# Kernel optimization log

Hardware: AMD Instinct MI355X
Metric: run time of the kernel (lower is better)

Reference implementation:

```python
import jax, jax.numpy as jnp
import numpy as np

B = 128; DIM_IN = 3; MAX_CYCLE = 50; NODES = 18
T = MAX_CYCLE * NODES          # cycle_size = 900
F1, F2 = 32, 64                # stgcn_filters
NCLS = 3
N = B * T                      # nodes seen by GATv2 = 115200
E = 12 * N                     # edges (avg degree 12)
EPS = 1e-5


def setup_inputs() -> dict:
    key = jax.random.key(0)
    keys = iter(jax.random.split(key, 48))
    def p(shape, scale=0.05):
        return jax.random.normal(next(keys), shape, jnp.float32) * scale
    inp = {}
    inp["x"] = jax.random.normal(next(keys), (B, DIM_IN, T), jnp.float32)
    inp["edge_index"] = jax.random.randint(next(keys), (2, E), 0, N)
    def block(pfx, cin, c):
        inp[pfx + "_tc1_w"] = p((c, cin, 5)); inp[pfx + "_tc1_b"] = p((c,))
        inp[pfx + "_wl"] = p((c, c)); inp[pfx + "_bl"] = p((c,))
        inp[pfx + "_wr"] = p((c, c)); inp[pfx + "_br"] = p((c,))
        inp[pfx + "_att"] = p((c,)); inp[pfx + "_gbias"] = p((c,))
        inp[pfx + "_bn_g"] = jnp.ones((c,), jnp.float32)
        inp[pfx + "_bn_b"] = jnp.zeros((c,), jnp.float32)
        inp[pfx + "_tc2_w"] = p((c, c, 5)); inp[pfx + "_tc2_b"] = p((c,))
    block("b1", DIM_IN, F1)
    block("b2", F1, F2)
    inp["fc1_w"] = p((128, T * F2), 0.01); inp["fc1_b"] = p((128,))
    inp["hbn1_g"] = jnp.ones((128,), jnp.float32); inp["hbn1_b"] = jnp.zeros((128,), jnp.float32)
    inp["fc2_w"] = p((64, 128)); inp["fc2_b"] = p((64,))
    inp["hbn2_g"] = jnp.ones((64,), jnp.float32); inp["hbn2_b"] = jnp.zeros((64,), jnp.float32)
    inp["fc3_w"] = p((NCLS, 64)); inp["fc3_b"] = p((NCLS,))
    return inp


def _conv1d_same(x, w, b):
    # x: [B, Cin, T], w: [Cout, Cin, 5], 'same' padding (pad 2/2)
    y = jax.lax.conv_general_dilated(x, w, (1,), [(2, 2)],
                                     dimension_numbers=("NCH", "OIH", "NCH"))
    return y + b[None, :, None]


def _bn(h, g, b):
    # BatchNorm1d on [N, C] with batch statistics
    m = h.mean(0)
    v = h.var(0)
    return (h - m) * jax.lax.rsqrt(v + EPS) * g + b


def _gatv2(h, src, dst, wl, bl, wr, br, att, gbias):
    # PyG GATv2Conv, heads=1, negative_slope=0.2, self loops already in src/dst
    xl = h @ wl.T + bl            # source transform, also the message
    xr = h @ wr.T + br            # target transform
    e = jnp.dot(jax.nn.leaky_relu(xl[src] + xr[dst], 0.2), att)  # [E]
    m = jax.ops.segment_max(e, dst, num_segments=N)
    ex = jnp.exp(e - m[dst])
    s = jax.ops.segment_sum(ex, dst, num_segments=N)
    alpha = ex / s[dst]
    out = jax.ops.segment_sum(alpha[:, None] * xl[src], dst, num_segments=N)
    return out + gbias


def _block(x, src, dst, tc1_w, tc1_b, wl, bl, wr, br, att, gbias, bn_g, bn_b, tc2_w, tc2_b):
    x = jax.nn.relu(_conv1d_same(x, tc1_w, tc1_b))      # [B, C, T]
    C = tc1_w.shape[0]
    h = x.reshape(T * B, C)                             # torch .view(T*B, C) (raw row-major)
    h = jax.nn.relu(_gatv2(h, src, dst, wl, bl, wr, br, att, gbias))
    h = _bn(h, bn_g, bn_b)
    h = h.reshape(B, C, T)                              # torch .view(B, C, T)
    return jax.nn.relu(_conv1d_same(h, tc2_w, tc2_b))


def reference(x, edge_index,
              b1_tc1_w, b1_tc1_b, b1_wl, b1_bl, b1_wr, b1_br, b1_att, b1_gbias,
              b1_bn_g, b1_bn_b, b1_tc2_w, b1_tc2_b,
              b2_tc1_w, b2_tc1_b, b2_wl, b2_bl, b2_wr, b2_br, b2_att, b2_gbias,
              b2_bn_g, b2_bn_b, b2_tc2_w, b2_tc2_b,
              fc1_w, fc1_b, hbn1_g, hbn1_b, fc2_w, fc2_b, hbn2_g, hbn2_b, fc3_w, fc3_b):
    sl = jnp.arange(N, dtype=edge_index.dtype)          # PyG add_self_loops=True
    src = jnp.concatenate([edge_index[0], sl])
    dst = jnp.concatenate([edge_index[1], sl])
    h = _block(x, src, dst, b1_tc1_w, b1_tc1_b, b1_wl, b1_bl, b1_wr, b1_br,
               b1_att, b1_gbias, b1_bn_g, b1_bn_b, b1_tc2_w, b1_tc2_b)
    h = jax.nn.relu(h)                                  # extra relu on non-final block (dropout off)
    h = _block(h, src, dst, b2_tc1_w, b2_tc1_b, b2_wl, b2_bl, b2_wr, b2_br,
               b2_att, b2_gbias, b2_bn_g, b2_bn_b, b2_tc2_w, b2_tc2_b)
    h = h.reshape(B, F2 * T)
    h = jax.nn.relu(h @ fc1_w.T + fc1_b)
    h = _bn(h, hbn1_g, hbn1_b)
    h = jax.nn.relu(h @ fc2_w.T + fc2_b)
    h = _bn(h, hbn2_g, hbn2_b)
    logits = h @ fc3_w.T + fc3_b
    return (jax.nn.sigmoid(logits), logits)
```

## Files before the change

kernel.cpp:

```cpp
#include <hip/hip_runtime.h>
#include <hip/hip_bf16.h>

typedef __hip_bfloat16 bf16;
typedef __attribute__((ext_vector_type(8))) short s16x8;
typedef __attribute__((ext_vector_type(4))) float f32x4;
#define DEV static __device__ __forceinline__

DEV float b2f(bf16 v){ return __bfloat162float(v); }
DEV bf16  f2b(float v){ return __float2bfloat16(v); }
DEV int   is_f32(const void* gones){ return ((const unsigned int*)gones)[0] == 0x3F800000u ? 1 : 0; }
DEV float ldin(const void* p, int f32, int i){
    return f32 ? ((const float*)p)[i] : __bfloat162float(((const bf16*)p)[i]);
}
DEV void unpk(unsigned u, float& a, float& b){
    a = __uint_as_float(u << 16);
    b = __uint_as_float(u & 0xffff0000u);
}
DEV float lrelu(float t){ return fmaxf(t, 0.f) + 0.2f * fminf(t, 0.f); }
DEV unsigned short bfu(float v){ bf16 h = f2b(v); return *(unsigned short*)&h; }

constexpr int Bb  = 128;
constexpr int Tt  = 900;
constexpr int Nn  = Bb * Tt;
constexpr int Ee  = 12 * Nn;
constexpr int CAP = 48;
constexpr int NBK  = 256;
constexpr int NPB  = Nn / NBK;
constexpr int BCAP = 8192;
constexpr int WROWS = 96 + 1024 + 2048 + 4096;
constexpr int WTOT  = WROWS * 5;
constexpr int WBF   = 5120 + 10240 + 20480;

__global__ __launch_bounds__(256) void k_wprep(const void* wa, const void* wb_, const void* wc,
    const void* wd, const void* gones, float* __restrict__ wp, bf16* __restrict__ wbf,
    int* __restrict__ gcur){
    const int f32 = is_f32(gones);
    if (blockIdx.x == 0 && threadIdx.x < NBK) gcur[threadIdx.x] = 0;
    int e = blockIdx.x * 256 + threadIdx.x;
    if (e < WTOT){
        int r = e / 5, k = e - r * 5;
        const void* src; int rb;
        if (r < 96)      { src = wa; rb = 0; }
        else if (r < 1120){ src = wb_; rb = 96; }
        else if (r < 3168){ src = wc; rb = 1120; }
        else             { src = wd; rb = 3168; }
        wp[r * 8 + k] = ldin(src, f32, (r - rb) * 5 + k);
    } else if (e < WTOT + WBF){
        int e2 = e - WTOT;
        const void* src; int kk, r;
        if (e2 < 5120)      { kk = e2 >> 10; r = e2 & 1023; src = wb_; }
        else if (e2 < 15360){ int e3 = e2 - 5120;  kk = e3 >> 11; r = e3 & 2047; src = wc; }
        else                { int e3 = e2 - 15360; kk = e3 >> 12; r = e3 & 4095; src = wd; }
        wbf[e2] = f2b(ldin(src, f32, r * 5 + kk));
    }
}

__global__ __launch_bounds__(256) void k_bucket(const int* __restrict__ ei,
                                                int* __restrict__ gcur, int2* __restrict__ bkt){
    constexpr int TILE = 4096;
    const int base = blockIdx.x * TILE;
    const int tid = threadIdx.x;
    __shared__ int cnt[NBK];
    __shared__ int gbase[NBK];
    cnt[tid] = 0;
    __syncthreads();
    int es[16], er[16], eb[16], rk[16];
    #pragma unroll
    for (int k = 0; k < 16; ++k){
        int idx = base + k * 256 + tid;
        if (idx < Ee){
            es[k] = ei[idx];
            int d = ei[Ee + idx];
            eb[k] = d / NPB;
            er[k] = d - eb[k] * NPB;
            rk[k] = atomicAdd(&cnt[eb[k]], 1);
        } else eb[k] = -1;
    }
    __syncthreads();
    {
        int c = cnt[tid];
        gbase[tid] = (c > 0) ? atomicAdd(&gcur[tid], c) : 0;
    }
    __syncthreads();
    #pragma unroll
    for (int k = 0; k < 16; ++k){
        if (eb[k] >= 0){
            int slot = gbase[eb[k]] + rk[k];
            if (slot < BCAP)
                bkt[(size_t)eb[k] * BCAP + slot] = make_int2(er[k], es[k]);
        }
    }
}

__global__ __launch_bounds__(256) void k_csr2(const int2* __restrict__ bkt, const int* __restrict__ gcur,
                                              int* __restrict__ csr, int* __restrict__ cnt){
    const int b = blockIdx.x;
    const int n0 = b * NPB;
    __shared__ int lcnt[NPB];
    for (int i = threadIdx.x; i < NPB; i += 256) lcnt[i] = 0;
    __syncthreads();
    const int tot = min(gcur[b], BCAP);
    for (int i = threadIdx.x; i < tot; i += 256){
        int2 e = bkt[(size_t)b * BCAP + i];
        int p = atomicAdd(&lcnt[e.x], 1);
        if (p < CAP) csr[(size_t)(n0 + e.x) * CAP + p] = e.y;
    }
    __syncthreads();
    for (int i = threadIdx.x; i < NPB; i += 256) cnt[n0 + i] = lcnt[i];
}

template<bool EXT, int CIN, int COUT, bool BN>
__global__ __launch_bounds__(256) void k_conv(const void* __restrict__ x,
    const float* __restrict__ wp, int wbase,
    const void* __restrict__ bias, const float* __restrict__ scale, const float* __restrict__ shift,
    const void* __restrict__ gones, float* __restrict__ y)
{
    const int f32 = is_f32(gones);
    __shared__ alignas(16) float xs[CIN][132];
    const int b = blockIdx.x >> 3, t0 = (blockIdx.x & 7) * 128;
    const int tid = threadIdx.x;
    for (int i = tid; i < CIN * 132; i += 256){
        int ci = i / 132, tt = i % 132;
        int gt = t0 + tt - 2;
        float v = 0.f;
        if (gt >= 0 && gt < Tt){
            int idx = (b * CIN + ci) * Tt + gt;
            v = EXT ? ldin(x, f32, idx) : ((const float*)x)[idx];
            if (BN){
                int f = (ci * (Tt % CIN) + gt) % CIN;
                v = v * scale[f] + shift[f];
            }
        }
        xs[ci][tt] = v;
    }
    __syncthreads();
    constexpr int HALF = COUT / 2;
    constexpr int NT   = 256 / HALF;
    constexpr int NW   = 128 / (NT * 4);
    const int cop = tid / NT;
    const int tch = tid % NT;
    const int co = cop, co2 = cop + HALF;
    float acc[NW][2][4];
    #pragma unroll
    for (int iw = 0; iw < NW; ++iw)
        #pragma unroll
        for (int h = 0; h < 2; ++h)
            #pragma unroll
            for (int j = 0; j < 4; ++j) acc[iw][h][j] = 0.f;

    const float* w0p = wp + (size_t)(wbase + co  * CIN) * 8;
    const float* w1p = wp + (size_t)(wbase + co2 * CIN) * 8;
    float4 na = *(const float4*)w0p; float na4 = w0p[4];
    float4 nb = *(const float4*)w1p; float nb4 = w1p[4];
    for (int ci = 0; ci < CIN; ++ci){
        const float w0[5] = {na.x, na.y, na.z, na.w, na4};
        const float w1[5] = {nb.x, nb.y, nb.z, nb.w, nb4};
        if (ci + 1 < CIN){
            const float* p0 = w0p + (size_t)(ci + 1) * 8;
            const float* p1 = w1p + (size_t)(ci + 1) * 8;
            na = *(const float4*)p0; na4 = p0[4];
            nb = *(const float4*)p1; nb4 = p1[4];
        }
        #pragma unroll
        for (int iw = 0; iw < NW; ++iw){
            const int tl = tch * 4 + iw * NT * 4;
            float4 a  = *(const float4*)&xs[ci][tl];
            float4 bq = *(const float4*)&xs[ci][tl + 4];
            float xw[8] = {a.x,a.y,a.z,a.w,bq.x,bq.y,bq.z,bq.w};
            #pragma unroll
            for (int k = 0; k < 5; ++k)
                #pragma unroll
                for (int j = 0; j < 4; ++j){
                    acc[iw][0][j] = fmaf(xw[j + k], w0[k], acc[iw][0][j]);
                    acc[iw][1][j] = fmaf(xw[j + k], w1[k], acc[iw][1][j]);
                }
        }
    }
    const float bv0 = ldin(bias, f32, co), bv1 = ldin(bias, f32, co2);
    #pragma unroll
    for (int iw = 0; iw < NW; ++iw){
        const int t = t0 + tch * 4 + iw * NT * 4;
        if (t < Tt){
            float4 o0, o1;
            o0.x = fmaxf(acc[iw][0][0] + bv0, 0.f); o0.y = fmaxf(acc[iw][0][1] + bv0, 0.f);
            o0.z = fmaxf(acc[iw][0][2] + bv0, 0.f); o0.w = fmaxf(acc[iw][0][3] + bv0, 0.f);
            o1.x = fmaxf(acc[iw][1][0] + bv1, 0.f); o1.y = fmaxf(acc[iw][1][1] + bv1, 0.f);
            o1.z = fmaxf(acc[iw][1][2] + bv1, 0.f); o1.w = fmaxf(acc[iw][1][3] + bv1, 0.f);
            *(float4*)&y[(b * COUT + co ) * Tt + t] = o0;
            *(float4*)&y[(b * COUT + co2) * Tt + t] = o1;
        }
    }
}

template<int CIN, int COUT, bool BN>
__global__ __launch_bounds__(256) void k_convM(const float* __restrict__ x, const bf16* __restrict__ wbf,
    int wbase,
    const void* __restrict__ bias, const float* __restrict__ scale, const float* __restrict__ shift,
    const void* __restrict__ gones, float* __restrict__ y)
{
    const int f32 = is_f32(gones);
    constexpr int STR = CIN + 8;
    constexpr int CI2 = CIN / 2;
    __shared__ alignas(16) float smem[COUT * 132];
    unsigned short* xsT = (unsigned short*)smem;
    const int b = blockIdx.x >> 3, t0 = (blockIdx.x & 7) * 128;
    const int tid = threadIdx.x;
    for (int i = tid; i < CI2 * 128; i += 256){
        int ci2 = i >> 7, tt = i & 127;
        int gt = t0 + tt - 2;
        int ci = ci2 * 2;
        unsigned pack = 0;
        if (gt >= 0 && gt < Tt){
            float v0 = x[(b * CIN + ci) * Tt + gt];
            float v1 = x[(b * CIN + ci + 1) * Tt + gt];
            if (BN){
                int fa = (4 * ci + gt) & (CIN - 1), fb = (4 * ci + 4 + gt) & (CIN - 1);
                v0 = v0 * scale[fa] + shift[fa];
                v1 = v1 * scale[fb] + shift[fb];
            }
            pack = (unsigned)bfu(v0) | ((unsigned)bfu(v1) << 16);
        }
        *(unsigned*)&xsT[tt * STR + ci] = pack;
    }
    if (tid < CI2 * 4){
        int ci2 = tid >> 2, tt = 128 + (tid & 3);
        int gt = t0 + tt - 2;
        int ci = ci2 * 2;
        unsigned pack = 0;
        if (gt < Tt){
            float v0 = x[(b * CIN + ci) * Tt + gt];
            float v1 = x[(b * CIN + ci + 1) * Tt + gt];
            if (BN){
                int fa = (4 * ci + gt) & (CIN - 1), fb = (4 * ci + 4 + gt) & (CIN - 1);
                v0 = v0 * scale[fa] + shift[fa];
                v1 = v1 * scale[fb] + shift[fb];
            }
            pack = (unsigned)bfu(v0) | ((unsigned)bfu(v1) << 16);
        }
        *(unsigned*)&xsT[tt * STR + ci] = pack;
    }
    __syncthreads();
    const int lane = tid & 63, wid = tid >> 6;
    const int l15 = lane & 15, quad = lane >> 4;
    constexpr int MT  = COUT / 16;
    constexpr int NTP = 2 * MT;
    const int mt  = (MT == 4) ? wid : (wid & 1);
    const int ntb = (MT == 4) ? 0 : (wid >> 1) * NTP;
    const int co0 = mt * 16;
    f32x4 acc[NTP];
    #pragma unroll
    for (int nt = 0; nt < NTP; ++nt){ f32x4 z = {0.f, 0.f, 0.f, 0.f}; acc[nt] = z; }
    for (int kk = 0; kk < 5; ++kk){
        #pragma unroll
        for (int kb = 0; kb < CIN / 32; ++kb){
            s16x8 a = *(const s16x8*)&wbf[wbase + kk * (COUT * CIN) + (co0 + l15) * CIN + kb * 32 + quad * 8];
            #pragma unroll
            for (int nt = 0; nt < NTP; ++nt){
                s16x8 bf = *(const s16x8*)&xsT[((ntb + nt) * 16 + l15 + kk) * STR + kb * 32 + quad * 8];
                acc[nt] = __builtin_amdgcn_mfma_f32_16x16x32_bf16(a, bf, acc[nt], 0, 0, 0);
            }
        }
    }
    __syncthreads();
    #pragma unroll
    for (int nt = 0; nt < NTP; ++nt)
        #pragma unroll
        for (int r = 0; r < 4; ++r)
            smem[(co0 + quad * 4 + r) * 132 + (ntb + nt) * 16 + l15] = acc[nt][r];
    __syncthreads();
    for (int i = tid; i < COUT * 32; i += 256){
        int co = i >> 5, c4 = (i & 31) << 2;
        int t = t0 + c4;
        if (t < Tt){
            float4 o = *(float4*)&smem[co * 132 + c4];
            float bb = ldin(bias, f32, co);
            o.x = fmaxf(o.x + bb, 0.f); o.y = fmaxf(o.y + bb, 0.f);
            o.z = fmaxf(o.z + bb, 0.f); o.w = fmaxf(o.w + bb, 0.f);
            float* dst = &y[(b * COUT + co) * Tt + t];
            if (t + 3 < Tt) *(float4*)dst = o;
            else {
                float ov[4] = {o.x, o.y, o.z, o.w};
                for (int j = 0; j < 4 && t + j < Tt; ++j) dst[j] = ov[j];
            }
        }
    }
}

template<int C>
__global__ __launch_bounds__(256) void k_xlxr(const float* __restrict__ h,
    const void* __restrict__ wl, const void* __restrict__ bl,
    const void* __restrict__ wr, const void* __restrict__ br,
    const void* __restrict__ gones, unsigned short* __restrict__ xlh, float* __restrict__ xr)
{
    const int f32 = is_f32(gones);
    constexpr int NB = 4096 / C;
    constexpr int HS = NB + 4;
    constexpr int WS = C + 4;
    __shared__ alignas(16) float hT [C][HS];
    __shared__ alignas(16) float wlT[C][WS];
    __shared__ alignas(16) float wrT[C][WS];
    const int tid = threadIdx.x;
    const int n0 = blockIdx.x * NB;
    for (int i = tid; i < NB * C; i += 256){
        int n = i / C, c = i % C;
        hT[c][n] = h[(n0 + n) * C + c];
    }
    for (int i = tid; i < C * C; i += 256){
        int f = i / C, c = i % C;
        wlT[c][f] = ldin(wl, f32, i);
        wrT[c][f] = ldin(wr, f32, i);
    }
    __syncthreads();
    constexpr int FG = C / 4;
    const int fg = tid % FG, ng = tid / FG;
    const int nloc = ng * 4, floc = fg * 4;
    float blv[4], brv[4];
    #pragma unroll
    for (int j = 0; j < 4; ++j){ blv[j] = ldin(bl, f32, floc + j); brv[j] = ldin(br, f32, floc + j); }
    float accL[4][4], accR[4][4];
    #pragma unroll
    for (int i = 0; i < 4; ++i)
        #pragma unroll
        for (int j = 0; j < 4; ++j){ accL[i][j] = 0.f; accR[i][j] = 0.f; }
    for (int c = 0; c < C; ++c){
        float4 hv = *(const float4*)&hT [c][nloc];
        float4 lv = *(const float4*)&wlT[c][floc];
        float4 rv = *(const float4*)&wrT[c][floc];
        float ha[4] = {hv.x,hv.y,hv.z,hv.w};
        float la[4] = {lv.x,lv.y,lv.z,lv.w};
        float ra[4] = {rv.x,rv.y,rv.z,rv.w};
        #pragma unroll
        for (int i = 0; i < 4; ++i)
            #pragma unroll
            for (int j = 0; j < 4; ++j){
                accL[i][j] = fmaf(ha[i], la[j], accL[i][j]);
                accR[i][j] = fmaf(ha[i], ra[j], accR[i][j]);
            }
    }
    #pragma unroll
    for (int i = 0; i < 4; ++i){
        size_t n = n0 + nloc + i;
        bf16 hb[4];
        hb[0] = f2b(accL[i][0] + blv[0]); hb[1] = f2b(accL[i][1] + blv[1]);
        hb[2] = f2b(accL[i][2] + blv[2]); hb[3] = f2b(accL[i][3] + blv[3]);
        *(ushort4*)&xlh[n * C + floc] = *(ushort4*)hb;
        float4 r;
        r.x = accR[i][0] + brv[0]; r.y = accR[i][1] + brv[1];
        r.z = accR[i][2] + brv[2]; r.w = accR[i][3] + brv[3];
        *(float4*)&xr[n * C + floc] = r;
    }
}

template<int L> DEV float rsumL(float v){
    #pragma unroll
    for (int s = L / 2; s > 0; s >>= 1) v += __shfl_xor(v, s, 64);
    return v;
}

template<int C, int FPL>
__global__ __launch_bounds__(256) void k_gat(const unsigned short* __restrict__ xlh,
    const float* __restrict__ xr,
    const int* __restrict__ csr, const int* __restrict__ cnt,
    const void* __restrict__ att, const void* __restrict__ gbias,
    const void* __restrict__ gones, float* __restrict__ out)
{
    const int f32 = is_f32(gones);
    constexpr int L   = C / FPL;
    constexpr int NPW = 64 / L;
    const int lane = threadIdx.x & 63, wid = threadIdx.x >> 6;
    const int sub = lane / L, fp = lane % L;
    const int node = (blockIdx.x * 4 + wid) * NPW + sub;
    const int f0 = FPL * fp;
    float xrv[FPL], attv[FPL];
    if constexpr (FPL == 4){
        float4 t = *(const float4*)&xr[(size_t)node * C + f0];
        xrv[0] = t.x; xrv[1] = t.y; xrv[2] = t.z; xrv[3] = t.w;
    } else {
        float2 t = *(const float2*)&xr[(size_t)node * C + f0];
        xrv[0] = t.x; xrv[1] = t.y;
    }
    #pragma unroll
    for (int i = 0; i < FPL; ++i) attv[i] = ldin(att, f32, f0 + i);
    const int deg = min(cnt[node], CAP);
    int degu = deg;
    degu = max(degu, __shfl_xor(degu, 32, 64));
    degu = max(degu, __shfl_xor(degu, 16, 64));

    auto loadv = [&](int s, float (&v)[FPL]){
        if constexpr (FPL == 4){
            uint2 u = *(const uint2*)&xlh[(size_t)s * C + f0];
            unpk(u.x, v[0], v[1]); unpk(u.y, v[2], v[3]);
        } else {
            unsigned u = *(const unsigned*)&xlh[(size_t)s * C + f0];
            unpk(u, v[0], v[1]);
        }
    };
    auto score = [&](const float (&v)[FPL]){
        float l = lrelu(v[0] + xrv[0]) * attv[0];
        #pragma unroll
        for (int i = 1; i < FPL; ++i) l = fmaf(lrelu(v[i] + xrv[i]), attv[i], l);
        return rsumL<L>(l);
    };

    float ssum, acc[FPL];
    {
        float v[FPL];
        loadv(node, v);
        float w = __expf(score(v));
        ssum = w;
        #pragma unroll
        for (int i = 0; i < FPL; ++i) acc[i] = w * v[i];
    }
    for (int j = 0; j < degu; j += 4){
        int4 s4 = *(const int4*)&csr[(size_t)node * CAP + j];
        const bool a0 = (j + 0 < deg), a1 = (j + 1 < deg), a2 = (j + 2 < deg), a3 = (j + 3 < deg);
        int s0 = a0 ? s4.x : node, s1 = a1 ? s4.y : node;
        int s2 = a2 ? s4.z : node, s3 = a3 ? s4.w : node;
        float v0[FPL], v1[FPL], v2[FPL], v3[FPL];
        loadv(s0, v0); loadv(s1, v1); loadv(s2, v2); loadv(s3, v3);
        float e0 = score(v0), e1 = score(v1), e2 = score(v2), e3 = score(v3);
        float w0 = a0 ? __expf(e0) : 0.f;
        float w1 = a1 ? __expf(e1) : 0.f;
        float w2 = a2 ? __expf(e2) : 0.f;
        float w3 = a3 ? __expf(e3) : 0.f;
        ssum += (w0 + w1) + (w2 + w3);
        #pragma unroll
        for (int i = 0; i < FPL; ++i)
            acc[i] += fmaf(w0, v0[i], w1 * v1[i]) + fmaf(w2, v2[i], w3 * v3[i]);
    }
    float inv = 1.f / ssum;
    if constexpr (FPL == 4){
        float4 o;
        o.x = fmaxf(fmaf(acc[0], inv, ldin(gbias, f32, f0)),     0.f);
        o.y = fmaxf(fmaf(acc[1], inv, ldin(gbias, f32, f0 + 1)), 0.f);
        o.z = fmaxf(fmaf(acc[2], inv, ldin(gbias, f32, f0 + 2)), 0.f);
        o.w = fmaxf(fmaf(acc[3], inv, ldin(gbias, f32, f0 + 3)), 0.f);
        *(float4*)&out[(size_t)node * C + f0] = o;
    } else {
        float2 o;
        o.x = fmaxf(fmaf(acc[0], inv, ldin(gbias, f32, f0)),     0.f);
        o.y = fmaxf(fmaf(acc[1], inv, ldin(gbias, f32, f0 + 1)), 0.f);
        *(float2*)&out[(size_t)node * C + f0] = o;
    }
}

template<int C>
__global__ __launch_bounds__(256) void k_bnstat1(const float* __restrict__ h, double* __restrict__ part){
    const int tid = threadIdx.x;
    double s1 = 0.0, s2 = 0.0;
    const int total = Nn * C;
    for (int idx = blockIdx.x * 256 + tid; idx < total; idx += 65536){
        float v = h[idx];
        s1 += v; s2 += (double)v * v;
    }
    __shared__ double r1[256], r2[256];
    r1[tid] = s1; r2[tid] = s2;
    __syncthreads();
    if (tid < C){
        double a = 0.0, b = 0.0;
        #pragma unroll
        for (int q = 0; q < 256 / C; ++q){ a += r1[tid + q * C]; b += r2[tid + q * C]; }
        part[blockIdx.x * 2 * C + tid]     = a;
        part[blockIdx.x * 2 * C + C + tid] = b;
    }
}

template<int C>
__global__ void k_bnstat2(const double* __restrict__ part, const void* __restrict__ g,
                          const void* __restrict__ b, const void* __restrict__ gones,
                          float* __restrict__ scale, float* __restrict__ shift){
    const int f32 = is_f32(gones);
    const int f = threadIdx.x;
    double s1 = 0.0, s2 = 0.0;
    for (int s = 0; s < 256; ++s){ s1 += part[s * 2 * C + f]; s2 += part[s * 2 * C + C + f]; }
    double mean = s1 / (double)Nn;
    double var  = s2 / (double)Nn - mean * mean;
    float sc = (float)((double)ldin(g, f32, f) / sqrt(var + 1e-5));
    float sh = ldin(b, f32, f) - (float)mean * sc;
    scale[f] = sc; shift[f] = sh;
}

__global__ __launch_bounds__(256) void k_fc1(const float* __restrict__ h, const void* __restrict__ w1,
                                             const void* __restrict__ gones, float* __restrict__ part){
    const int f32 = is_f32(gones);
    __shared__ alignas(16) float AT[32][136];
    __shared__ alignas(16) float BT[32][136];
    const int tid = threadIdx.x;
    const int blk = blockIdx.x;
    const int k0 = blk * 128;
    const int bg = tid >> 4, jg = tid & 15;
    const int row = tid >> 5, kk = tid & 31;
    float ar[16], br[16];
    #pragma unroll
    for (int q = 0; q < 16; ++q){
        int idx = (row + q * 8) * 57600 + k0 + kk;
        ar[q] = h[idx];
        br[q] = ldin(w1, f32, idx);
    }
    float acc[8][8];
    #pragma unroll
    for (int i = 0; i < 8; ++i)
        #pragma unroll
        for (int j = 0; j < 8; ++j) acc[i][j] = 0.f;
    for (int ch = 0; ch < 4; ++ch){
        __syncthreads();
        #pragma unroll
        for (int q = 0; q < 16; ++q){
            AT[kk][row + q * 8] = ar[q];
            BT[kk][row + q * 8] = br[q];
        }
        __syncthreads();
        if (ch < 3){
            const int kb = k0 + (ch + 1) * 32;
            #pragma unroll
            for (int q = 0; q < 16; ++q){
                int idx = (row + q * 8) * 57600 + kb + kk;
                ar[q] = h[idx];
                br[q] = ldin(w1, f32, idx);
            }
        }
        for (int k2 = 0; k2 < 32; ++k2){
            float4 a0 = *(const float4*)&AT[k2][bg * 8];
            float4 a1 = *(const float4*)&AT[k2][bg * 8 + 4];
            float4 c0 = *(const float4*)&BT[k2][jg * 8];
            float4 c1 = *(const float4*)&BT[k2][jg * 8 + 4];
            float av[8] = {a0.x,a0.y,a0.z,a0.w,a1.x,a1.y,a1.z,a1.w};
            float bv[8] = {c0.x,c0.y,c0.z,c0.w,c1.x,c1.y,c1.z,c1.w};
            #pragma unroll
            for (int i = 0; i < 8; ++i)
                #pragma unroll
                for (int j = 0; j < 8; ++j) acc[i][j] = fmaf(av[i], bv[j], acc[i][j]);
        }
    }
    #pragma unroll
    for (int i = 0; i < 8; ++i){
        int bb = bg * 8 + i;
        #pragma unroll
        for (int q = 0; q < 2; ++q){
            float4 o;
            o.x = acc[i][q*4+0]; o.y = acc[i][q*4+1]; o.z = acc[i][q*4+2]; o.w = acc[i][q*4+3];
            *(float4*)&part[blk * 16384 + bb * 128 + jg * 8 + q * 4] = o;
        }
    }
}

__global__ void k_fc1red1(const float* __restrict__ part, float* __restrict__ pr2){
    const int y = blockIdx.x >> 6;
    const int o = (blockIdx.x & 63) * 256 + threadIdx.x;
    const int sb0 = y * 57;
    const int sb1 = min(sb0 + 57, 450);
    float s = 0.f;
    for (int sb = sb0; sb < sb1; ++sb) s += part[(size_t)sb * 16384 + o];
    pr2[(size_t)y * 16384 + o] = s;
}

__global__ void k_fc1red2(const float* __restrict__ pr2, const void* __restrict__ bias,
                          const void* __restrict__ gones, float* __restrict__ out1){
    const int f32 = is_f32(gones);
    const int o = blockIdx.x * 256 + threadIdx.x;
    float s = ldin(bias, f32, o & 127);
    #pragma unroll
    for (int y = 0; y < 8; ++y) s += pr2[(size_t)y * 16384 + o];
    out1[o] = fmaxf(s, 0.f);
}

__global__ void k_hstat(const float* __restrict__ out1, const void* __restrict__ g1,
                        const void* __restrict__ b1, const void* __restrict__ gones,
                        float* __restrict__ sc, float* __restrict__ sh){
    const int f32 = is_f32(gones);
    const int f = threadIdx.x;
    double s1 = 0.0, s2 = 0.0;
    for (int r = 0; r < 128; ++r){ float v = out1[r * 128 + f]; s1 += v; s2 += (double)v * v; }
    double mean = s1 / 128.0, var = s2 / 128.0 - mean * mean;
    float s = (float)((double)ldin(g1, f32, f) / sqrt(var + 1e-5));
    sc[f] = s;
    sh[f] = ldin(b1, f32, f) - (float)mean * s;
}

__global__ __launch_bounds__(256) void k_fc2(const float* __restrict__ out1,
    const float* __restrict__ sc, const float* __restrict__ sh,
    const void* __restrict__ w2, const void* __restrict__ fb2,
    const void* __restrict__ gones, float* __restrict__ f2)
{
    const int f32 = is_f32(gones);
    __shared__ alignas(16) float hs[4 * 128];
    __shared__ alignas(16) float w2s[64 * 132];
    const int tid = threadIdx.x;
    const int b0 = blockIdx.x * 4;
    for (int i = tid; i < 512; i += 256){
        int f = i & 127;
        hs[i] = out1[b0 * 128 + i] * sc[f] + sh[f];
    }
    for (int i = tid; i < 8192; i += 256)
        w2s[(i >> 7) * 132 + (i & 127)] = ldin(w2, f32, i);
    __syncthreads();
    const int b = tid >> 6, o = tid & 63;
    float acc = ldin(fb2, f32, o);
    const float* hp = &hs[b * 128];
    const float* wq = &w2s[o * 132];
    #pragma unroll
    for (int k = 0; k < 128; k += 4){
        float4 hv = *(const float4*)&hp[k];
        float4 wv = *(const float4*)&wq[k];
        acc = fmaf(hv.x, wv.x, acc); acc = fmaf(hv.y, wv.y, acc);
        acc = fmaf(hv.z, wv.z, acc); acc = fmaf(hv.w, wv.w, acc);
    }
    f2[(b0 + b) * 64 + o] = fmaxf(acc, 0.f);
}

__global__ __launch_bounds__(256) void k_head2(const float* __restrict__ f2,
    const void* g2, const void* b2v, const void* w3, const void* fb3,
    const void* gones, void* __restrict__ out)
{
    const int f32 = is_f32(gones);
    __shared__ float fs[8192];
    __shared__ float sc2[64], sh2[64];
    const int tid = threadIdx.x;
    for (int i = tid; i < 8192; i += 256) fs[i] = f2[i];
    __syncthreads();
    if (tid < 64){
        double s1 = 0.0, s2 = 0.0;
        for (int r = 0; r < 128; ++r){ float v = fs[r * 64 + tid]; s1 += v; s2 += (double)v * v; }
        double mean = s1 / 128.0, var = s2 / 128.0 - mean * mean;
        sc2[tid] = (float)((double)ldin(g2, f32, tid) / sqrt(var + 1e-5));
        sh2[tid] = ldin(b2v, f32, tid) - (float)mean * sc2[tid];
    }
    __syncthreads();
    if (tid < 128){
        float hv[64];
        for (int k = 0; k < 64; ++k) hv[k] = fs[tid * 64 + k] * sc2[k] + sh2[k];
        #pragma unroll
        for (int c = 0; c < 3; ++c){
            float acc = ldin(fb3, f32, c);
            for (int k = 0; k < 64; ++k) acc = fmaf(hv[k], ldin(w3, f32, c * 64 + k), acc);
            float sg = 1.f / (1.f + __expf(-acc));
            if (f32){
                ((float*)out)[384 + tid * 3 + c] = acc;
                ((float*)out)[tid * 3 + c] = sg;
            } else {
                ((bf16*)out)[384 + tid * 3 + c] = f2b(acc);
                ((bf16*)out)[tid * 3 + c] = f2b(sg);
            }
        }
    }
}

extern "C" void kernel_launch(void* const* d_in, const int* in_sizes, int n_in,
                              void* d_out, int out_size, void* d_ws, size_t ws_size,
                              hipStream_t stream)
{
    const void* x   = d_in[0];
    const int*  ei  = (const int*)d_in[1];
    const void* b1_tc1_w=d_in[2];  const void* b1_tc1_b=d_in[3];
    const void* b1_wl   =d_in[4];  const void* b1_bl   =d_in[5];
    const void* b1_wr   =d_in[6];  const void* b1_br   =d_in[7];
    const void* b1_att  =d_in[8];  const void* b1_gb   =d_in[9];
    const void* b1_g    =d_in[10]; const void* b1_bt   =d_in[11];
    const void* b1_tc2_w=d_in[12]; const void* b1_tc2_b=d_in[13];
    const void* b2_tc1_w=d_in[14]; const void* b2_tc1_b=d_in[15];
    const void* b2_wl   =d_in[16]; const void* b2_bl   =d_in[17];
    const void* b2_wr   =d_in[18]; const void* b2_br   =d_in[19];
    const void* b2_att  =d_in[20]; const void* b2_gb   =d_in[21];
    const void* b2_g    =d_in[22]; const void* b2_bt   =d_in[23];
    const void* b2_tc2_w=d_in[24]; const void* b2_tc2_b=d_in[25];
    const void* fc1_w=d_in[26]; const void* fc1_b=d_in[27];
    const void* hbn1_g=d_in[28]; const void* hbn1_b=d_in[29];
    const void* fc2_w=d_in[30]; const void* fc2_b=d_in[31];
    const void* hbn2_g=d_in[32]; const void* hbn2_b=d_in[33];
    const void* fc3_w=d_in[34]; const void* fc3_b=d_in[35];
    const void* gones = b1_g;

    float* ws = (float*)d_ws;
    const size_t NC = (size_t)Nn * 64;
    float* buf0 = ws;
    float* buf1 = ws + NC;
    float* buf2 = ws + 2 * NC;
    int*   csr  = (int*)(ws + 3 * NC);
    int*   cnt  = (int*)((char*)csr + (size_t)Nn * CAP * 4);
    double* bnp = (double*)((char*)cnt + (size_t)Nn * 4);
    float* scale = (float*)(bnp + 32768);
    float* shift = scale + 128;
    unsigned short* xlh = (unsigned short*)(shift + 128);
    int*   gcur = (int*)(xlh + (size_t)Nn * 64);
    float* wp   = (float*)(gcur + NBK);
    bf16*  wbf  = (bf16*)(wp + (size_t)WROWS * 8);
    int2*  bkt  = (int2*)buf2;
    float* part = buf0;
    float* out1 = buf2;
    float* pr2  = buf2 + 16384;
    float* f2b_ = pr2 + 8 * 16384;
    float* hsc  = f2b_ + 8192;
    float* hsh  = hsc + 128;

    k_wprep <<<(WTOT + WBF + 255) / 256, 256, 0, stream>>>(b1_tc1_w, b1_tc2_w, b2_tc1_w, b2_tc2_w,
                                                           gones, wp, wbf, gcur);
    k_bucket<<<(Ee + 4095) / 4096, 256, 0, stream>>>(ei, gcur, bkt);
    k_csr2  <<<NBK, 256, 0, stream>>>(bkt, gcur, csr, cnt);

    k_conv<true, 3, 32, false><<<Bb * 8, 256, 0, stream>>>(x, wp, 0, b1_tc1_b, nullptr, nullptr, gones, buf0);
    k_xlxr<32><<<Nn / 128, 256, 0, stream>>>(buf0, b1_wl, b1_bl, b1_wr, b1_br, gones, xlh, buf1);
    k_gat<32, 2><<<Nn / 16, 256, 0, stream>>>(xlh, buf1, csr, cnt, b1_att, b1_gb, gones, buf2);
    k_bnstat1<32><<<256, 256, 0, stream>>>(buf2, bnp);
    k_bnstat2<32><<<1, 32, 0, stream>>>(bnp, b1_g, b1_bt, gones, scale, shift);
    k_convM<32, 32, true><<<Bb * 8, 256, 0, stream>>>(buf2, wbf, 0, b1_tc2_b, scale, shift, gones, buf0);

    k_convM<32, 64, false><<<Bb * 8, 256, 0, stream>>>(buf0, wbf, 5120, b2_tc1_b, nullptr, nullptr, gones, buf1);
    k_xlxr<64><<<Nn / 64, 256, 0, stream>>>(buf1, b2_wl, b2_bl, b2_wr, b2_br, gones, xlh, buf2);
    k_gat<64, 4><<<Nn / 16, 256, 0, stream>>>(xlh, buf2, csr, cnt, b2_att, b2_gb, gones, buf0);
    k_bnstat1<64><<<256, 256, 0, stream>>>(buf0, bnp);
    k_bnstat2<64><<<1, 64, 0, stream>>>(bnp, b2_g, b2_bt, gones, scale, shift);
    k_convM<64, 64, true><<<Bb * 8, 256, 0, stream>>>(buf0, wbf, 15360, b2_tc2_b, scale, shift, gones, buf1);

    k_fc1<<<450, 256, 0, stream>>>(buf1, fc1_w, gones, part);
    k_fc1red1<<<512, 256, 0, stream>>>(part, pr2);
    k_fc1red2<<<64, 256, 0, stream>>>(pr2, fc1_b, gones, out1);
    k_hstat<<<1, 128, 0, stream>>>(out1, hbn1_g, hbn1_b, gones, hsc, hsh);
    k_fc2<<<32, 256, 0, stream>>>(out1, hsc, hsh, fc2_w, fc2_b, gones, f2b_);
    k_head2<<<1, 256, 0, stream>>>(f2b_, hbn2_g, hbn2_b, fc3_w, fc3_b, gones, d_out);
}
```

Measured before the change: 539.9 us.

## Rewrite xl/xr projection as one-node-per-thread with preconverted fp32 weights

The GATv2 source/target projection kernel now gives each thread one node, holds its feature row in registers, and reads the weights from a global fp32 buffer with a wave-uniform access pattern instead of staging transposed tiles in shared memory. The weight-prep kernel gains a section that converts wl/wr/bl/br for both blocks into that buffer, so the per-block dtype checks and shared-memory setup go away. For C=64 the output features are split over two blocks to limit register pressure. The risk is uncoalesced per-thread row loads and stores with a node stride, and a higher register count.

```diff
diff --git a/kernel.cpp b/kernel.cpp
--- a/kernel.cpp
+++ b/kernel.cpp
@@ -30,10 +30,14 @@
 constexpr int WROWS = 96 + 1024 + 2048 + 4096;
 constexpr int WTOT  = WROWS * 5;
 constexpr int WBF   = 5120 + 10240 + 20480;
+constexpr int WXT   = 2*32*32 + 64 + 2*64*64 + 128;
 
 __global__ __launch_bounds__(256) void k_wprep(const void* wa, const void* wb_, const void* wc,
-    const void* wd, const void* gones, float* __restrict__ wp, bf16* __restrict__ wbf,
-    int* __restrict__ gcur){
+    const void* wd,
+    const void* b1wl, const void* b1bl, const void* b1wr, const void* b1br,
+    const void* b2wl, const void* b2bl, const void* b2wr, const void* b2br,
+    const void* gones, float* __restrict__ wp, bf16* __restrict__ wbf,
+    float* __restrict__ wx, int* __restrict__ gcur){
     const int f32 = is_f32(gones);
     if (blockIdx.x == 0 && threadIdx.x < NBK) gcur[threadIdx.x] = 0;
     int e = blockIdx.x * 256 + threadIdx.x;
@@ -52,6 +56,18 @@
         else if (e2 < 15360){ int e3 = e2 - 5120;  kk = e3 >> 11; r = e3 & 2047; src = wc; }
         else                { int e3 = e2 - 15360; kk = e3 >> 12; r = e3 & 4095; src = wd; }
         wbf[e2] = f2b(ldin(src, f32, r * 5 + kk));
+    } else if (e < WTOT + WBF + WXT){
+        int e3 = e - WTOT - WBF;
+        float v;
+        if      (e3 < 1024)  v = ldin(b1wl, f32, e3);
+        else if (e3 < 2048)  v = ldin(b1wr, f32, e3 - 1024);
+        else if (e3 < 2080)  v = ldin(b1bl, f32, e3 - 2048);
+        else if (e3 < 2112)  v = ldin(b1br, f32, e3 - 2080);
+        else if (e3 < 6208)  v = ldin(b2wl, f32, e3 - 2112);
+        else if (e3 < 10304) v = ldin(b2wr, f32, e3 - 6208);
+        else if (e3 < 10368) v = ldin(b2bl, f32, e3 - 10304);
+        else                 v = ldin(b2br, f32, e3 - 10368);
+        wx[e3] = v;
     }
 }
 
@@ -286,68 +302,50 @@
     }
 }
 
-template<int C>
+template<int C, int SPLIT>
 __global__ __launch_bounds__(256) void k_xlxr(const float* __restrict__ h,
-    const void* __restrict__ wl, const void* __restrict__ bl,
-    const void* __restrict__ wr, const void* __restrict__ br,
-    const void* __restrict__ gones, unsigned short* __restrict__ xlh, float* __restrict__ xr)
+    const float* __restrict__ wx, int wxoff,
+    unsigned short* __restrict__ xlh, float* __restrict__ xr)
 {
-    const int f32 = is_f32(gones);
-    constexpr int NB = 4096 / C;
-    constexpr int HS = NB + 4;
-    constexpr int WS = C + 4;
-    __shared__ alignas(16) float hT [C][HS];
-    __shared__ alignas(16) float wlT[C][WS];
-    __shared__ alignas(16) float wrT[C][WS];
-    const int tid = threadIdx.x;
-    const int n0 = blockIdx.x * NB;
-    for (int i = tid; i < NB * C; i += 256){
-        int n = i / C, c = i % C;
-        hT[c][n] = h[(n0 + n) * C + c];
-    }
-    for (int i = tid; i < C * C; i += 256){
-        int f = i / C, c = i % C;
-        wlT[c][f] = ldin(wl, f32, i);
-        wrT[c][f] = ldin(wr, f32, i);
-    }
-    __syncthreads();
-    constexpr int FG = C / 4;
-    const int fg = tid % FG, ng = tid / FG;
-    const int nloc = ng * 4, floc = fg * 4;
-    float blv[4], brv[4];
-    #pragma unroll
-    for (int j = 0; j < 4; ++j){ blv[j] = ldin(bl, f32, floc + j); brv[j] = ldin(br, f32, floc + j); }
-    float accL[4][4], accR[4][4];
-    #pragma unroll
-    for (int i = 0; i < 4; ++i)
-        #pragma unroll
-        for (int j = 0; j < 4; ++j){ accL[i][j] = 0.f; accR[i][j] = 0.f; }
-    for (int c = 0; c < C; ++c){
-        float4 hv = *(const float4*)&hT [c][nloc];
-        float4 lv = *(const float4*)&wlT[c][floc];
-        float4 rv = *(const float4*)&wrT[c][floc];
-        float ha[4] = {hv.x,hv.y,hv.z,hv.w};
-        float la[4] = {lv.x,lv.y,lv.z,lv.w};
-        float ra[4] = {rv.x,rv.y,rv.z,rv.w};
-        #pragma unroll
-        for (int i = 0; i < 4; ++i)
+    constexpr int NF = C / SPLIT;
+    const int node = (int)(blockIdx.x / SPLIT) * 256 + threadIdx.x;
+    const int fb   = (int)(blockIdx.x % SPLIT) * NF;
+    const float* wl = wx + wxoff;
+    const float* wr = wl + C * C;
+    const float* bl = wr + C * C;
+    const float* br = bl + C;
+    float hr[C];
+    #pragma unroll
+    for (int c4 = 0; c4 < C / 4; ++c4)
+        *(float4*)&hr[c4 * 4] = *(const float4*)&h[(size_t)node * C + c4 * 4];
+    for (int f0 = 0; f0 < NF; f0 += 4){
+        float oL[4], oR[4];
+        #pragma unroll
+        for (int j = 0; j < 4; ++j){
+            const int f = fb + f0 + j;
+            const float* wlr = wl + f * C;
+            const float* wrr = wr + f * C;
+            float a0 = 0.f, a1 = 0.f, a2 = 0.f, a3 = 0.f;
+            float r0 = 0.f, r1 = 0.f, r2 = 0.f, r3 = 0.f;
             #pragma unroll
-            for (int j = 0; j < 4; ++j){
-                accL[i][j] = fmaf(ha[i], la[j], accL[i][j]);
-                accR[i][j] = fmaf(ha[i], ra[j], accR[i][j]);
+            for (int c = 0; c < C; c += 4){
+                a0 = fmaf(hr[c],     wlr[c],     a0);
+                a1 = fmaf(hr[c + 1], wlr[c + 1], a1);
+                a2 = fmaf(hr[c + 2], wlr[c + 2], a2);
+                a3 = fmaf(hr[c + 3], wlr[c + 3], a3);
+                r0 = fmaf(hr[c],     wrr[c],     r0);
+                r1 = fmaf(hr[c + 1], wrr[c + 1], r1);
+                r2 = fmaf(hr[c + 2], wrr[c + 2], r2);
+                r3 = fmaf(hr[c + 3], wrr[c + 3], r3);
             }
-    }
-    #pragma unroll
-    for (int i = 0; i < 4; ++i){
-        size_t n = n0 + nloc + i;
-        bf16 hb[4];
-        hb[0] = f2b(accL[i][0] + blv[0]); hb[1] = f2b(accL[i][1] + blv[1]);
-        hb[2] = f2b(accL[i][2] + blv[2]); hb[3] = f2b(accL[i][3] + blv[3]);
-        *(ushort4*)&xlh[n * C + floc] = *(ushort4*)hb;
-        float4 r;
-        r.x = accR[i][0] + brv[0]; r.y = accR[i][1] + brv[1];
-        r.z = accR[i][2] + brv[2]; r.w = accR[i][3] + brv[3];
-        *(float4*)&xr[n * C + floc] = r;
+            oL[j] = ((a0 + a1) + (a2 + a3)) + bl[f];
+            oR[j] = ((r0 + r1) + (r2 + r3)) + br[f];
+        }
+        unsigned short hb[4];
+        hb[0] = bfu(oL[0]); hb[1] = bfu(oL[1]); hb[2] = bfu(oL[2]); hb[3] = bfu(oL[3]);
+        *(ushort4*)&xlh[(size_t)node * C + fb + f0] = *(ushort4*)hb;
+        float4 o; o.x = oR[0]; o.y = oR[1]; o.z = oR[2]; o.w = oR[3];
+        *(float4*)&xr[(size_t)node * C + fb + f0] = o;
     }
 }
 
@@ -684,6 +682,7 @@
     int*   gcur = (int*)(xlh + (size_t)Nn * 64);
     float* wp   = (float*)(gcur + NBK);
     bf16*  wbf  = (bf16*)(wp + (size_t)WROWS * 8);
+    float* wx   = (float*)(wbf + WBF);
     int2*  bkt  = (int2*)buf2;
     float* part = buf0;
     float* out1 = buf2;
@@ -692,20 +691,22 @@
     float* hsc  = f2b_ + 8192;
     float* hsh  = hsc + 128;
 
-    k_wprep <<<(WTOT + WBF + 255) / 256, 256, 0, stream>>>(b1_tc1_w, b1_tc2_w, b2_tc1_w, b2_tc2_w,
-                                                           gones, wp, wbf, gcur);
+    k_wprep <<<(WTOT + WBF + WXT + 255) / 256, 256, 0, stream>>>(
+        b1_tc1_w, b1_tc2_w, b2_tc1_w, b2_tc2_w,
+        b1_wl, b1_bl, b1_wr, b1_br, b2_wl, b2_bl, b2_wr, b2_br,
+        gones, wp, wbf, wx, gcur);
     k_bucket<<<(Ee + 4095) / 4096, 256, 0, stream>>>(ei, gcur, bkt);
     k_csr2  <<<NBK, 256, 0, stream>>>(bkt, gcur, csr, cnt);
 
     k_conv<true, 3, 32, false><<<Bb * 8, 256, 0, stream>>>(x, wp, 0, b1_tc1_b, nullptr, nullptr, gones, buf0);
-    k_xlxr<32><<<Nn / 128, 256, 0, stream>>>(buf0, b1_wl, b1_bl, b1_wr, b1_br, gones, xlh, buf1);
+    k_xlxr<32, 1><<<Nn / 256, 256, 0, stream>>>(buf0, wx, 0, xlh, buf1);
     k_gat<32, 2><<<Nn / 16, 256, 0, stream>>>(xlh, buf1, csr, cnt, b1_att, b1_gb, gones, buf2);
     k_bnstat1<32><<<256, 256, 0, stream>>>(buf2, bnp);
     k_bnstat2<32><<<1, 32, 0, stream>>>(bnp, b1_g, b1_bt, gones, scale, shift);
     k_convM<32, 32, true><<<Bb * 8, 256, 0, stream>>>(buf2, wbf, 0, b1_tc2_b, scale, shift, gones, buf0);
 
     k_convM<32, 64, false><<<Bb * 8, 256, 0, stream>>>(buf0, wbf, 5120, b2_tc1_b, nullptr, nullptr, gones, buf1);
-    k_xlxr<64><<<Nn / 64, 256, 0, stream>>>(buf1, b2_wl, b2_bl, b2_wr, b2_br, gones, xlh, buf2);
+    k_xlxr<64, 2><<<(Nn / 256) * 2, 256, 0, stream>>>(buf1, wx, 2112, xlh, buf2);
     k_gat<64, 4><<<Nn / 16, 256, 0, stream>>>(xlh, buf2, csr, cnt, b2_att, b2_gb, gones, buf0);
     k_bnstat1<64><<<256, 256, 0, stream>>>(buf0, bnp);
     k_bnstat2<64><<<1, 64, 0, stream>>>(bnp, b2_g, b2_bt, gones, scale, shift);
```

New measurement: 803.4 us. 48.8% more time.
